# Kernel tuning notes

Hardware: AMD Instinct MI355X
Metric: run time of the kernel (lower is better)

The kernel has to match this reference:

```python
import jax, jax.numpy as jnp
import numpy as np

N_NODES = 100000
N_EDGES = 800000
DIM_E = 64
HEAD = 4


def setup_inputs() -> dict:
    key = jax.random.key(0)
    ks = jax.random.split(key, 6)
    embeds = jax.random.normal(ks[0], (N_NODES, DIM_E), dtype=jnp.float32)
    Wq = jax.random.normal(ks[1], (DIM_E, DIM_E), dtype=jnp.float32) * (1.0 / np.sqrt(DIM_E))
    Wk = jax.random.normal(ks[2], (DIM_E, DIM_E), dtype=jnp.float32) * (1.0 / np.sqrt(DIM_E))
    Wv = jax.random.normal(ks[3], (DIM_E, DIM_E), dtype=jnp.float32) * (1.0 / np.sqrt(DIM_E))
    rows = jax.random.randint(ks[4], (N_EDGES,), 0, N_NODES, dtype=jnp.int32)
    cols = jax.random.randint(ks[5], (N_EDGES,), 0, N_NODES, dtype=jnp.int32)
    return {"embeds": embeds, "Wq": Wq, "Wk": Wk, "Wv": Wv, "rows": rows, "cols": cols}


def reference(embeds, Wq, Wk, Wv, rows, cols):
    H, D = HEAD, DIM_E
    Dh = D // H
    E = rows.shape[0]
    rowE = embeds[rows]                     # [E, D] gather
    colE = embeds[cols]                     # [E, D] gather
    q = (rowE @ Wq).reshape(E, H, Dh)
    k = (colE @ Wk).reshape(E, H, Dh)
    v = (colE @ Wv).reshape(E, H, Dh)
    att = jnp.clip(jnp.einsum('ehd,ehd->eh', q, k), -10.0, 10.0)
    expAtt = jnp.exp(att)                   # [E, H]
    # segment softmax: scatter-add per destination row, gather back
    attNorm = jax.ops.segment_sum(expAtt, rows, num_segments=N_NODES)[rows]
    att = expAtt / (attNorm + 1e-8)         # [E, H]
    res = (att[:, :, None] * v).reshape(E, D)
    res = jax.ops.segment_sum(res, rows, num_segments=N_NODES)  # [N, D]
    return (res, att)
```

## Files before the change

### kernel.cpp

```cpp
#include <hip/hip_runtime.h>

#define N_NODES 100000
#define N_EDGES 800000
#define DIM 64
#define HEADS 4

#define SCAN_BLK 256
#define N_SCAN_BLOCKS ((N_NODES + SCAN_BLK - 1) / SCAN_BLK)

typedef __attribute__((ext_vector_type(8))) short bf16x8;
typedef __attribute__((ext_vector_type(4))) float f32x4;

__device__ __forceinline__ short f2bf(float x) {
    union { float f; unsigned u; } v; v.f = x;
    unsigned r = (v.u + 0x7FFFu + ((v.u >> 16) & 1u)) >> 16;
    return (short)r;
}
__device__ __forceinline__ float bf2f(short b) {
    union { float f; unsigned u; } v; v.u = ((unsigned)(unsigned short)b) << 16;
    return v.f;
}

__global__ __launch_bounds__(256) void wprep_kernel(
    const float* __restrict__ Wq, const float* __restrict__ Wk,
    const float* __restrict__ Wv,
    short* __restrict__ wfragH, short* __restrict__ wfragL)
{
    const int idx = blockIdx.x * 256 + threadIdx.x;
    if (idx >= 12288) return;
    const int j    = idx & 7;
    const int lane = (idx >> 3) & 63;
    const int kt   = (idx >> 9) & 1;
    const int nt   = idx >> 10;
    const int k      = kt * 32 + (lane >> 4) * 8 + j;
    const int col192 = nt * 16 + (lane & 15);
    const float* W = (col192 < 64) ? Wq : ((col192 < 128) ? Wk : Wv);
    const float x = W[k * DIM + (col192 & 63)];
    const short hb = f2bf(x);
    wfragH[idx] = hb;
    wfragL[idx] = f2bf(x - bf2f(hb));
}

__global__ __launch_bounds__(256) void qkv_mfma_kernel(
    const float* __restrict__ embeds,
    const short* __restrict__ wfragH,
    const short* __restrict__ wfragL,
    float* __restrict__ Q, float* __restrict__ K, float* __restrict__ V)
{
    __shared__ __align__(16) short sBH[12288];
    __shared__ __align__(16) short sBL[12288];

    const int t = threadIdx.x;
    {
        const int4* srcH = (const int4*)wfragH;
        const int4* srcL = (const int4*)wfragL;
        int4* dH = (int4*)sBH; int4* dL = (int4*)sBL;
        #pragma unroll
        for (int i = 0; i < 6; ++i) {
            dH[t + 256 * i] = srcH[t + 256 * i];
            dL[t + 256 * i] = srcL[t + 256 * i];
        }
    }
    __syncthreads();

    const int lane = t & 63;
    const int wid  = t >> 6;
    const int m0 = blockIdx.x * 64 + wid * 16;

    int arow = m0 + (lane & 15);
    if (arow >= N_NODES) arow = N_NODES - 1;
    const float* ap = embeds + (size_t)arow * DIM + ((lane >> 4) * 8);

    bf16x8 aH[2], aL[2];
    #pragma unroll
    for (int kt = 0; kt < 2; ++kt) {
        const float4 x0 = ((const float4*)(ap + kt * 32))[0];
        const float4 x1 = ((const float4*)(ap + kt * 32))[1];
        const float xs[8] = {x0.x, x0.y, x0.z, x0.w, x1.x, x1.y, x1.z, x1.w};
        bf16x8 h8, l8;
        #pragma unroll
        for (int j = 0; j < 8; ++j) {
            const short hb = f2bf(xs[j]);
            h8[j] = hb;
            l8[j] = f2bf(xs[j] - bf2f(hb));
        }
        aH[kt] = h8; aL[kt] = l8;
    }

    f32x4 acc[12];
    #pragma unroll
    for (int nt = 0; nt < 12; ++nt) acc[nt] = (f32x4){0.f, 0.f, 0.f, 0.f};

    #pragma unroll
    for (int kt = 0; kt < 2; ++kt) {
        #pragma unroll
        for (int nt = 0; nt < 12; ++nt) {
            const int o = ((nt * 2 + kt) * 64 + lane) * 8;
            const bf16x8 bH = *(const bf16x8*)(sBH + o);
            const bf16x8 bL = *(const bf16x8*)(sBL + o);
            acc[nt] = __builtin_amdgcn_mfma_f32_16x16x32_bf16(aH[kt], bH, acc[nt], 0, 0, 0);
            acc[nt] = __builtin_amdgcn_mfma_f32_16x16x32_bf16(aH[kt], bL, acc[nt], 0, 0, 0);
            acc[nt] = __builtin_amdgcn_mfma_f32_16x16x32_bf16(aL[kt], bH, acc[nt], 0, 0, 0);
        }
    }

    const int rbase = m0 + (lane >> 4) * 4;
    const int cl = lane & 15;
    #pragma unroll
    for (int nt = 0; nt < 12; ++nt) {
        const int col192 = nt * 16 + cl;
        float* dst = (col192 < 64) ? Q : ((col192 < 128) ? K : V);
        const int c = col192 & 63;
        #pragma unroll
        for (int r = 0; r < 4; ++r) {
            const int row = rbase + r;
            if (row < N_NODES) dst[(size_t)row * DIM + c] = acc[nt][r];
        }
    }
}

__global__ __launch_bounds__(256) void hist_kernel(
    const int* __restrict__ rows, int* __restrict__ counts)
{
    const int e = blockIdx.x * 256 + threadIdx.x;
    if (e < N_EDGES) atomicAdd(&counts[rows[e]], 1);
}

__global__ __launch_bounds__(SCAN_BLK) void scanA_kernel(
    const int* __restrict__ counts, int* __restrict__ blockSums)
{
    __shared__ int tile[SCAN_BLK];
    const int i = blockIdx.x * SCAN_BLK + threadIdx.x;
    tile[threadIdx.x] = (i < N_NODES) ? counts[i] : 0;
    __syncthreads();
    for (int off = SCAN_BLK / 2; off > 0; off >>= 1) {
        if (threadIdx.x < off) tile[threadIdx.x] += tile[threadIdx.x + off];
        __syncthreads();
    }
    if (threadIdx.x == 0) blockSums[blockIdx.x] = tile[0];
}

__global__ __launch_bounds__(512) void scanB_kernel(int* __restrict__ blockSums)
{
    __shared__ int s[512];
    const int t = threadIdx.x;
    const int v = (t < N_SCAN_BLOCKS) ? blockSums[t] : 0;
    s[t] = v;
    __syncthreads();
    for (int off = 1; off < 512; off <<= 1) {
        const int add = (t >= off) ? s[t - off] : 0;
        __syncthreads();
        s[t] += add;
        __syncthreads();
    }
    if (t < N_SCAN_BLOCKS) blockSums[t] = s[t] - v;
}

__global__ __launch_bounds__(SCAN_BLK) void scanC_kernel(
    const int* __restrict__ counts,
    const int* __restrict__ blockSums,
    int* __restrict__ offsets,
    int* __restrict__ cursor)
{
    __shared__ int tile[SCAN_BLK];
    const int i = blockIdx.x * SCAN_BLK + threadIdx.x;
    const int v = (i < N_NODES) ? counts[i] : 0;
    tile[threadIdx.x] = v;
    __syncthreads();
    for (int off = 1; off < SCAN_BLK; off <<= 1) {
        const int add = (threadIdx.x >= off) ? tile[threadIdx.x - off] : 0;
        __syncthreads();
        tile[threadIdx.x] += add;
        __syncthreads();
    }
    if (i < N_NODES) {
        const int excl = tile[threadIdx.x] - v + blockSums[blockIdx.x];
        offsets[i] = excl;
        cursor[i]  = excl;
    }
}

__global__ __launch_bounds__(256) void scatter_kernel(
    const int* __restrict__ rows,
    const int* __restrict__ cols,
    int* __restrict__ cursor,
    int2* __restrict__ sortedPair)
{
    const int e = blockIdx.x * 256 + threadIdx.x;
    if (e < N_EDGES) {
        const int r = rows[e];
        const int pos = atomicAdd(&cursor[r], 1);
        sortedPair[pos] = make_int2(cols[e], e);
    }
}

__global__ __launch_bounds__(256) void node_agg_kernel(
    const float* __restrict__ Q,
    const float* __restrict__ K,
    const float* __restrict__ V,
    const int* __restrict__ offsets,
    const int* __restrict__ counts,
    const int2* __restrict__ sortedPair,
    float* __restrict__ attOut,
    float* __restrict__ normArr,
    float* __restrict__ res)
{
    const int node = (blockIdx.x * 256 + threadIdx.x) >> 6;
    const int lane = threadIdx.x & 63;
    if (node >= N_NODES) return;

    const int start = offsets[node];
    const int cnt   = counts[node];

    const int slot = lane >> 2;
    const int h    = lane & 3;
    const int hd   = lane >> 4;

    const float4* qp = (const float4*)(Q + (size_t)node * DIM + h * 16);
    const float4 q0 = qp[0], q1 = qp[1], q2 = qp[2], q3 = qp[3];

    float normacc = 0.0f;
    float acc     = 0.0f;

    for (int cb = 0; cb < cnt; cb += 16) {
        const int jj = cb + slot;
        const bool active = (jj < cnt);
        int2 pr = make_int2(0, 0);
        if (active) pr = sortedPair[start + jj];
        const int col = pr.x;

        const float4* kp = (const float4*)(K + (size_t)col * DIM + h * 16);
        const float4 k0 = kp[0], k1 = kp[1], k2 = kp[2], k3 = kp[3];
        float s = q0.x*k0.x + q0.y*k0.y + q0.z*k0.z + q0.w*k0.w
                + q1.x*k1.x + q1.y*k1.y + q1.z*k1.z + q1.w*k1.w
                + q2.x*k2.x + q2.y*k2.y + q2.z*k2.z + q2.w*k2.w
                + q3.x*k3.x + q3.y*k3.y + q3.z*k3.z + q3.w*k3.w;
        s = fminf(fmaxf(s, -10.0f), 10.0f);
        const float ex = active ? __expf(s) : 0.0f;
        if (active) attOut[(size_t)pr.y * HEADS + h] = ex;
        normacc += ex;

        float vv[16];
        #pragma unroll
        for (int s2 = 0; s2 < 16; ++s2) {
            const int c2 = __builtin_amdgcn_readlane(col, s2 * 4);
            vv[s2] = V[(size_t)c2 * DIM + lane];
        }
        #pragma unroll
        for (int s2 = 0; s2 < 16; ++s2) {
            acc = fmaf(__shfl(ex, s2 * 4 + hd, 64), vv[s2], acc);
        }
    }

    #pragma unroll
    for (int m2 = 4; m2 <= 32; m2 <<= 1)
        normacc += __shfl_xor(normacc, m2, 64);

    if (lane < 4) normArr[(size_t)node * HEADS + lane] = normacc;

    const float nrm = __shfl(normacc, hd, 64);
    res[(size_t)node * DIM + lane] = acc / (nrm + 1e-8f);
}

__global__ __launch_bounds__(256) void norm_edge_kernel(
    const int* __restrict__ rows,
    const float* __restrict__ normArr,
    float* __restrict__ attOut)
{
    const int tid = blockIdx.x * 256 + threadIdx.x;
    const int e = tid >> 2, h = tid & 3;
    if (e >= N_EDGES) return;
    const float ex = attOut[tid];
    const int r = rows[e];
    attOut[tid] = ex / (normArr[(size_t)r * HEADS + h] + 1e-8f);
}


extern "C" void kernel_launch(void* const* d_in, const int* in_sizes, int n_in,
                              void* d_out, int out_size, void* d_ws, size_t ws_size,
                              hipStream_t stream) {
    const float* embeds = (const float*)d_in[0];
    const float* Wq     = (const float*)d_in[1];
    const float* Wk     = (const float*)d_in[2];
    const float* Wv     = (const float*)d_in[3];
    const int*   rows   = (const int*)d_in[4];
    const int*   cols   = (const int*)d_in[5];

    float* out    = (float*)d_out;
    float* res    = out;
    float* attOut = out + (size_t)N_NODES * DIM;

    float* Q         = (float*)d_ws;
    float* K         = Q + (size_t)N_NODES * DIM;
    float* V         = K + (size_t)N_NODES * DIM;
    int*   counts    = (int*)(V + (size_t)N_NODES * DIM);
    int*   offsets   = counts + N_NODES;
    int*   cursor    = offsets + N_NODES;
    int2*  sortedPair= (int2*)(cursor + N_NODES);
    int*   blockSums = (int*)(sortedPair + N_EDGES);
    short* wfragH    = (short*)(blockSums + 512);
    short* wfragL    = wfragH + 12288;
    float* normArr   = (float*)(wfragL + 12288);

    hipMemsetAsync(counts, 0, (size_t)N_NODES * sizeof(int), stream);

    wprep_kernel<<<48, 256, 0, stream>>>(Wq, Wk, Wv, wfragH, wfragL);
    qkv_mfma_kernel<<<(N_NODES + 63) / 64, 256, 0, stream>>>(embeds, wfragH, wfragL, Q, K, V);

    const int eblocks = (N_EDGES + 255) / 256;
    hist_kernel<<<eblocks, 256, 0, stream>>>(rows, counts);
    scanA_kernel<<<N_SCAN_BLOCKS, SCAN_BLK, 0, stream>>>(counts, blockSums);
    scanB_kernel<<<1, 512, 0, stream>>>(blockSums);
    scanC_kernel<<<N_SCAN_BLOCKS, SCAN_BLK, 0, stream>>>(counts, blockSums, offsets, cursor);
    scatter_kernel<<<eblocks, 256, 0, stream>>>(rows, cols, cursor, sortedPair);

    const int nblocks = (N_NODES * 64 + 255) / 256;
    node_agg_kernel<<<nblocks, 256, 0, stream>>>(Q, K, V, offsets, counts,
                                                 sortedPair, attOut, normArr, res);

    const int hblocks = (N_EDGES * HEADS + 255) / 256;
    norm_edge_kernel<<<hblocks, 256, 0, stream>>>(rows, normArr, attOut);
}
```

Before: 283.0 us.

## Store K/V in bf16, replace scatter atomics with hist ranks, vectorize edge norm

K and V projections are now stored as bf16 rather than fp32, which halves the bytes fetched by the random gathers in the node aggregation kernel. The histogram kernel records each edge's rank within its row, so the scatter step computes positions as offset plus rank instead of using a second atomic pass. The edge-normalisation kernel now handles all four heads of an edge with float4 loads. Keeping K and V in bf16 lowers the precision of the attention scores and of the aggregated values, and the rank array needs extra workspace.

```diff
diff --git a/kernel.cpp b/kernel.cpp
--- a/kernel.cpp
+++ b/kernel.cpp
@@ -45,7 +45,9 @@
     const float* __restrict__ embeds,
     const short* __restrict__ wfragH,
     const short* __restrict__ wfragL,
-    float* __restrict__ Q, float* __restrict__ K, float* __restrict__ V)
+    float* __restrict__ Q,
+    unsigned short* __restrict__ Kb,
+    unsigned short* __restrict__ Vb)
 {
     __shared__ __align__(16) short sBH[12288];
     __shared__ __align__(16) short sBL[12288];
@@ -109,21 +111,27 @@
     #pragma unroll
     for (int nt = 0; nt < 12; ++nt) {
         const int col192 = nt * 16 + cl;
-        float* dst = (col192 < 64) ? Q : ((col192 < 128) ? K : V);
-        const int c = col192 & 63;
         #pragma unroll
         for (int r = 0; r < 4; ++r) {
             const int row = rbase + r;
-            if (row < N_NODES) dst[(size_t)row * DIM + c] = acc[nt][r];
+            if (row < N_NODES) {
+                if (col192 < 64)
+                    Q[(size_t)row * DIM + col192] = acc[nt][r];
+                else if (col192 < 128)
+                    Kb[(size_t)row * DIM + (col192 - 64)] = (unsigned short)f2bf(acc[nt][r]);
+                else
+                    Vb[(size_t)row * DIM + (col192 - 128)] = (unsigned short)f2bf(acc[nt][r]);
+            }
         }
     }
 }
 
 __global__ __launch_bounds__(256) void hist_kernel(
-    const int* __restrict__ rows, int* __restrict__ counts)
+    const int* __restrict__ rows, int* __restrict__ counts,
+    int* __restrict__ rank)
 {
     const int e = blockIdx.x * 256 + threadIdx.x;
-    if (e < N_EDGES) atomicAdd(&counts[rows[e]], 1);
+    if (e < N_EDGES) rank[e] = atomicAdd(&counts[rows[e]], 1);
 }
 
 __global__ __launch_bounds__(SCAN_BLK) void scanA_kernel(
@@ -159,8 +167,7 @@
 __global__ __launch_bounds__(SCAN_BLK) void scanC_kernel(
     const int* __restrict__ counts,
     const int* __restrict__ blockSums,
-    int* __restrict__ offsets,
-    int* __restrict__ cursor)
+    int* __restrict__ offsets)
 {
     __shared__ int tile[SCAN_BLK];
     const int i = blockIdx.x * SCAN_BLK + threadIdx.x;
@@ -173,31 +180,27 @@
         tile[threadIdx.x] += add;
         __syncthreads();
     }
-    if (i < N_NODES) {
-        const int excl = tile[threadIdx.x] - v + blockSums[blockIdx.x];
-        offsets[i] = excl;
-        cursor[i]  = excl;
-    }
+    if (i < N_NODES) offsets[i] = tile[threadIdx.x] - v + blockSums[blockIdx.x];
 }
 
 __global__ __launch_bounds__(256) void scatter_kernel(
     const int* __restrict__ rows,
     const int* __restrict__ cols,
-    int* __restrict__ cursor,
+    const int* __restrict__ offsets,
+    const int* __restrict__ rank,
     int2* __restrict__ sortedPair)
 {
     const int e = blockIdx.x * 256 + threadIdx.x;
     if (e < N_EDGES) {
-        const int r = rows[e];
-        const int pos = atomicAdd(&cursor[r], 1);
+        const int pos = offsets[rows[e]] + rank[e];
         sortedPair[pos] = make_int2(cols[e], e);
     }
 }
 
 __global__ __launch_bounds__(256) void node_agg_kernel(
     const float* __restrict__ Q,
-    const float* __restrict__ K,
-    const float* __restrict__ V,
+    const unsigned short* __restrict__ Kb,
+    const unsigned short* __restrict__ Vb,
     const int* __restrict__ offsets,
     const int* __restrict__ counts,
     const int2* __restrict__ sortedPair,
@@ -216,8 +219,12 @@
     const int h    = lane & 3;
     const int hd   = lane >> 4;
 
-    const float4* qp = (const float4*)(Q + (size_t)node * DIM + h * 16);
-    const float4 q0 = qp[0], q1 = qp[1], q2 = qp[2], q3 = qp[3];
+    float qv[16];
+    {
+        const float4* qp = (const float4*)(Q + (size_t)node * DIM + h * 16);
+        ((float4*)qv)[0] = qp[0]; ((float4*)qv)[1] = qp[1];
+        ((float4*)qv)[2] = qp[2]; ((float4*)qv)[3] = qp[3];
+    }
 
     float normacc = 0.0f;
     float acc     = 0.0f;
@@ -229,26 +236,29 @@
         if (active) pr = sortedPair[start + jj];
         const int col = pr.x;
 
-        const float4* kp = (const float4*)(K + (size_t)col * DIM + h * 16);
-        const float4 k0 = kp[0], k1 = kp[1], k2 = kp[2], k3 = kp[3];
-        float s = q0.x*k0.x + q0.y*k0.y + q0.z*k0.z + q0.w*k0.w
-                + q1.x*k1.x + q1.y*k1.y + q1.z*k1.z + q1.w*k1.w
-                + q2.x*k2.x + q2.y*k2.y + q2.z*k2.z + q2.w*k2.w
-                + q3.x*k3.x + q3.y*k3.y + q3.z*k3.z + q3.w*k3.w;
+        const unsigned short* kp = Kb + (size_t)col * DIM + h * 16;
+        const bf16x8 k0 = *(const bf16x8*)kp;
+        const bf16x8 k1 = *(const bf16x8*)(kp + 8);
+        float s = 0.0f;
+        #pragma unroll
+        for (int j = 0; j < 8; ++j) s = fmaf(qv[j], bf2f(k0[j]), s);
+        #pragma unroll
+        for (int j = 0; j < 8; ++j) s = fmaf(qv[8 + j], bf2f(k1[j]), s);
+
         s = fminf(fmaxf(s, -10.0f), 10.0f);
         const float ex = active ? __expf(s) : 0.0f;
         if (active) attOut[(size_t)pr.y * HEADS + h] = ex;
         normacc += ex;
 
-        float vv[16];
+        unsigned short raw[16];
         #pragma unroll
         for (int s2 = 0; s2 < 16; ++s2) {
             const int c2 = __builtin_amdgcn_readlane(col, s2 * 4);
-            vv[s2] = V[(size_t)c2 * DIM + lane];
+            raw[s2] = Vb[(size_t)c2 * DIM + lane];
         }
         #pragma unroll
         for (int s2 = 0; s2 < 16; ++s2) {
-            acc = fmaf(__shfl(ex, s2 * 4 + hd, 64), vv[s2], acc);
+            acc = fmaf(__shfl(ex, s2 * 4 + hd, 64), bf2f((short)raw[s2]), acc);
         }
     }
 
@@ -267,12 +277,15 @@
     const float* __restrict__ normArr,
     float* __restrict__ attOut)
 {
-    const int tid = blockIdx.x * 256 + threadIdx.x;
-    const int e = tid >> 2, h = tid & 3;
+    const int e = blockIdx.x * 256 + threadIdx.x;
     if (e >= N_EDGES) return;
-    const float ex = attOut[tid];
-    const int r = rows[e];
-    attOut[tid] = ex / (normArr[(size_t)r * HEADS + h] + 1e-8f);
+    float4 ex4 = ((const float4*)attOut)[e];
+    const float4 n4 = ((const float4*)normArr)[rows[e]];
+    ex4.x /= (n4.x + 1e-8f);
+    ex4.y /= (n4.y + 1e-8f);
+    ex4.z /= (n4.z + 1e-8f);
+    ex4.w /= (n4.w + 1e-8f);
+    ((float4*)attOut)[e] = ex4;
 }
 
 
@@ -290,34 +303,33 @@
     float* res    = out;
     float* attOut = out + (size_t)N_NODES * DIM;
 
-    float* Q         = (float*)d_ws;
-    float* K         = Q + (size_t)N_NODES * DIM;
-    float* V         = K + (size_t)N_NODES * DIM;
-    int*   counts    = (int*)(V + (size_t)N_NODES * DIM);
-    int*   offsets   = counts + N_NODES;
-    int*   cursor    = offsets + N_NODES;
-    int2*  sortedPair= (int2*)(cursor + N_NODES);
-    int*   blockSums = (int*)(sortedPair + N_EDGES);
-    short* wfragH    = (short*)(blockSums + 512);
-    short* wfragL    = wfragH + 12288;
-    float* normArr   = (float*)(wfragL + 12288);
+    float*          Q         = (float*)d_ws;
+    unsigned short* Kb        = (unsigned short*)(Q + (size_t)N_NODES * DIM);
+    unsigned short* Vb        = Kb + (size_t)N_NODES * DIM;
+    int2*           sortedPair= (int2*)(Vb + (size_t)N_NODES * DIM);
+    int*            counts    = (int*)(sortedPair + N_EDGES);
+    int*            offsets   = counts + N_NODES;
+    int*            rank      = offsets + N_NODES;
+    int*            blockSums = rank + N_EDGES;
+    short*          wfragH    = (short*)(blockSums + 512);
+    short*          wfragL    = wfragH + 12288;
+    float*          normArr   = (float*)(wfragL + 12288);
 
     hipMemsetAsync(counts, 0, (size_t)N_NODES * sizeof(int), stream);
 
     wprep_kernel<<<48, 256, 0, stream>>>(Wq, Wk, Wv, wfragH, wfragL);
-    qkv_mfma_kernel<<<(N_NODES + 63) / 64, 256, 0, stream>>>(embeds, wfragH, wfragL, Q, K, V);
+    qkv_mfma_kernel<<<(N_NODES + 63) / 64, 256, 0, stream>>>(embeds, wfragH, wfragL, Q, Kb, Vb);
 
     const int eblocks = (N_EDGES + 255) / 256;
-    hist_kernel<<<eblocks, 256, 0, stream>>>(rows, counts);
+    hist_kernel<<<eblocks, 256, 0, stream>>>(rows, counts, rank);
     scanA_kernel<<<N_SCAN_BLOCKS, SCAN_BLK, 0, stream>>>(counts, blockSums);
     scanB_kernel<<<1, 512, 0, stream>>>(blockSums);
-    scanC_kernel<<<N_SCAN_BLOCKS, SCAN_BLK, 0, stream>>>(counts, blockSums, offsets, cursor);
-    scatter_kernel<<<eblocks, 256, 0, stream>>>(rows, cols, cursor, sortedPair);
+    scanC_kernel<<<N_SCAN_BLOCKS, SCAN_BLK, 0, stream>>>(counts, blockSums, offsets);
+    scatter_kernel<<<eblocks, 256, 0, stream>>>(rows, cols, offsets, rank, sortedPair);
 
     const int nblocks = (N_NODES * 64 + 255) / 256;
-    node_agg_kernel<<<nblocks, 256, 0, stream>>>(Q, K, V, offsets, counts,
+    node_agg_kernel<<<nblocks, 256, 0, stream>>>(Q, Kb, Vb, offsets, counts,
                                                  sortedPair, attOut, normArr, res);
 
-    const int hblocks = (N_EDGES * HEADS + 255) / 256;
-    norm_edge_kernel<<<hblocks, 256, 0, stream>>>(rows, normArr, attOut);
-}
+    norm_edge_kernel<<<eblocks, 256, 0, stream>>>(rows, normArr, attOut);
+}
```

Result: faster. 231.5 us (-18.2%).
